# Optimization experiments

Measured on AMD Instinct MI355X. Metric: run time of the kernel, lower is better.

The kernel has to match this reference:

```python
import jax, jax.numpy as jnp
import numpy as np

S = 64   # feature-map height/width = sqrt(qvk_dim)
M = 2    # memory_block_size


def _block_divide(t):
    # (b, c, S*S) -> (b, c, (S/M)**2, M*M), matching
    # Rearrange('b c (h m1) (w m2) -> b c (h w) (m1 m2)')
    b, c, _ = t.shape
    h = S // M
    t = t.reshape(b, c, h, M, h, M)
    t = jnp.transpose(t, (0, 1, 2, 4, 3, 5))
    return t.reshape(b, c, h * h, M * M)


def setup_inputs() -> dict:
    key = jax.random.key(0)
    k1, k2, k3, k4 = jax.random.split(key, 4)
    B, C, F = 64, 64, S * S
    x = jax.random.normal(k1, (B, C, F), dtype=jnp.float32)
    scale = 1.0 / np.sqrt(F)
    Wq = jax.random.normal(k2, (F, F), dtype=jnp.float32) * scale
    Wk = jax.random.normal(k3, (F, F), dtype=jnp.float32) * scale
    Wv = jax.random.normal(k4, (F, F), dtype=jnp.float32) * scale
    return {"x": x, "Wq": Wq, "Wk": Wk, "Wv": Wv}


def reference(x, Wq, Wk, Wv):
    # Linear(in, out, bias=False): y = x @ W.T, W: (out, in)
    q = _block_divide(jnp.einsum('bcf,qf->bcq', x, Wq))  # (b,c,n,g)
    k = _block_divide(jnp.einsum('bcf,qf->bcq', x, Wk))  # (b,c,n,p)
    v = _block_divide(jnp.einsum('bcf,qf->bcq', x, Wv))  # (b,c,n,p)
    # score[b,c,n,g,p] = q[b,c,n,g] * k[b,c,n,p]; softmax over p (dim=4)
    score = q[..., :, None] * k[..., None, :]             # (b,c,n,g,p)
    att = jax.nn.softmax(score, axis=-1)
    # matmul(att (g,p), v (p,1)) -> (g,1), then flatten blocks
    out = jnp.einsum('bcngp,bcnp->bcng', att, v)          # (b,c,n,g)
    b, c, n, g = out.shape
    return out.reshape(b, c, n * g)
```

## Files before the change

### kernel.cpp

```cpp
#include <hip/hip_runtime.h>

#define F        4096
#define NE       ((size_t)F * F)

typedef __attribute__((ext_vector_type(8)))  short bf16x8;
typedef __attribute__((ext_vector_type(4)))  float f32x4;
typedef __attribute__((ext_vector_type(16))) float f32x16;

typedef const void __attribute__((address_space(1)))* gas1p;
typedef void __attribute__((address_space(3)))*       as3p;

__device__ __forceinline__ void gload16(const void* g, void* l) {
    __builtin_amdgcn_global_load_lds((gas1p)g, (as3p)l, 16, 0, 0);
}

__device__ __forceinline__ unsigned short f2bf(float f) {
    union { float f; unsigned int u; } c; c.f = f;
    unsigned int u = c.u;
    u += 0x7fffu + ((u >> 16) & 1u);
    return (unsigned short)(u >> 16);
}
__device__ __forceinline__ float bf2f(unsigned short u) {
    union { unsigned int u; float f; } c; c.u = ((unsigned int)u) << 16;
    return c.f;
}

__global__ void cvt_all(const float* __restrict__ s0, const float* __restrict__ s1,
                        const float* __restrict__ s2, const float* __restrict__ s3,
                        unsigned short* __restrict__ d0, unsigned short* __restrict__ d1,
                        unsigned short* __restrict__ d2, unsigned short* __restrict__ d3,
                        int n4) {
    const float* src = (blockIdx.y == 0) ? s0 : (blockIdx.y == 1) ? s1
                      : (blockIdx.y == 2) ? s2 : s3;
    unsigned short* dst = (blockIdx.y == 0) ? d0 : (blockIdx.y == 1) ? d1
                         : (blockIdx.y == 2) ? d2 : d3;
    int idx    = blockIdx.x * blockDim.x + threadIdx.x;
    int stride = gridDim.x * blockDim.x;
    const float4* in4 = (const float4*)src;
    ushort4* out4 = (ushort4*)dst;
    for (int i = idx; i < n4; i += stride) {
        float4 v = in4[i];
        ushort4 o;
        o.x = f2bf(v.x); o.y = f2bf(v.y); o.z = f2bf(v.z); o.w = f2bf(v.w);
        out4[i] = o;
    }
}

__device__ __forceinline__ int qo_map(int o) {
    int nblk = o >> 2, g = o & 3;
    return (nblk >> 5) * 128 + (g >> 1) * 64 + (nblk & 31) * 2 + (g & 1);
}

#define MFMA16(a, b, c) __builtin_amdgcn_mfma_f32_16x16x32_bf16(a, b, c, 0, 0, 0)
#define MFMA32(a, b, c) __builtin_amdgcn_mfma_f32_32x32x16_bf16(a, b, c, 0, 0, 0)

#define GBM 256
#define GBN 256
#define GBK 32
#define NKT (F / GBK)
#define ELPS (GBM * GBK)

__launch_bounds__(512, 1)
__global__ void gemm_qkv(const unsigned short* __restrict__ Xb,
                         const unsigned short* __restrict__ Qw,
                         const unsigned short* __restrict__ Kw,
                         const unsigned short* __restrict__ Vw,
                         unsigned short* __restrict__ qkv) {
    __shared__ __align__(16) unsigned short Als[4][GBM][GBK];
    __shared__ __align__(16) unsigned short Bls[4][GBN][GBK];

    const int tid  = threadIdx.x;
    const int lane = tid & 63;
    const int wid  = tid >> 6;
    const int wm   = wid >> 2;
    const int wn   = wid & 3;

    const int bid = blockIdx.x;
    const int swz = (bid & 7) * 96 + (bid >> 3);
    const int mt  = swz & 15;
    const int nt  = swz >> 4;
    const int bm  = mt * GBM;
    const int bnG = nt * GBN;
    const int mat = bnG >> 12;
    const int bn  = bnG & 4095;
    const unsigned short* __restrict__ Wsel = (mat == 0) ? Qw : (mat == 1) ? Kw : Vw;

    const int sr_row = tid >> 2;
    const int sr_chn = (tid & 3) ^ ((tid >> 3) & 3) ^ ((tid >> 5) & 3);
    const unsigned short* aSrc0 = Xb + (size_t)(bm + sr_row) * F + sr_chn * 8;
    const unsigned short* aSrc1 = aSrc0 + (size_t)128 * F;
    const unsigned short* bSrc0 = Wsel + (size_t)qo_map(bn + sr_row) * F + sr_chn * 8;
    const unsigned short* bSrc1 = Wsel + (size_t)qo_map(bn + 128 + sr_row) * F + sr_chn * 8;

#define STAGE_A(s, tt) do {                                                     \
        gload16(aSrc0 + (size_t)(tt) * GBK, (void*)&Als[s][wid * 16][0]);       \
        gload16(aSrc1 + (size_t)(tt) * GBK, (void*)&Als[s][128 + wid * 16][0]); \
    } while (0)
#define STAGE_B(s, tt) do {                                                     \
        gload16(bSrc0 + (size_t)(tt) * GBK, (void*)&Bls[s][wid * 16][0]);       \
        gload16(bSrc1 + (size_t)(tt) * GBK, (void*)&Bls[s][128 + wid * 16][0]); \
    } while (0)

    const int lrow = lane & 31;
    const int l5   = lane >> 5;
    const int rx   = ((lrow >> 1) & 3) ^ ((lrow >> 3) & 3);
    const int se0  = ((0 * 2 + l5) ^ rx) * 8;
    const int se1  = ((1 * 2 + l5) ^ rx) * 8;

    const unsigned short* aRow[4];
#pragma unroll
    for (int mi = 0; mi < 4; ++mi)
        aRow[mi] = &Als[0][wm * 128 + mi * 32 + lrow][0];
    const unsigned short* bRow[2];
#pragma unroll
    for (int nj = 0; nj < 2; ++nj)
        bRow[nj] = &Bls[0][wn * 64 + nj * 32 + lrow][0];

    f32x16 acc[4][2];
#pragma unroll
    for (int mi = 0; mi < 4; ++mi)
#pragma unroll
        for (int nj = 0; nj < 2; ++nj)
#pragma unroll
            for (int r = 0; r < 16; ++r)
                acc[mi][nj][r] = 0.f;

    STAGE_A(0, 0); STAGE_B(0, 0);
    STAGE_A(1, 1); STAGE_B(1, 1);
    STAGE_A(2, 2); STAGE_B(2, 2);
    asm volatile("s_waitcnt vmcnt(4)" ::: "memory");
    __builtin_amdgcn_s_barrier();
    __builtin_amdgcn_sched_barrier(0);

    bf16x8 af0[4], af1[4], bf0[2], bf1[2];
#pragma unroll
    for (int mi = 0; mi < 4; ++mi) {
        af0[mi] = *(const bf16x8*)(aRow[mi] + se0);
        af1[mi] = *(const bf16x8*)(aRow[mi] + se1);
    }
#pragma unroll
    for (int nj = 0; nj < 2; ++nj) {
        bf0[nj] = *(const bf16x8*)(bRow[nj] + se0);
        bf1[nj] = *(const bf16x8*)(bRow[nj] + se1);
    }

#pragma unroll 2
    for (int t = 0; t < NKT; ++t) {
        const int sn = (t + 1) & 3;
        const int ss = (t + 3) & 3;
        const int tt = (t + 3) & (NKT - 1);
        const int so = sn * ELPS;

        __builtin_amdgcn_s_setprio(1);
#pragma unroll
        for (int mi = 0; mi < 4; ++mi) {
            acc[mi][0] = MFMA32(af0[mi], bf0[0], acc[mi][0]);
            acc[mi][1] = MFMA32(af0[mi], bf0[1], acc[mi][1]);
            af0[mi] = *(const bf16x8*)(aRow[mi] + so + se0);
        }
        bf0[0] = *(const bf16x8*)(bRow[0] + so + se0);
        bf0[1] = *(const bf16x8*)(bRow[1] + so + se0);
#pragma unroll
        for (int mi = 0; mi < 4; ++mi) {
            acc[mi][0] = MFMA32(af1[mi], bf1[0], acc[mi][0]);
            acc[mi][1] = MFMA32(af1[mi], bf1[1], acc[mi][1]);
            af1[mi] = *(const bf16x8*)(aRow[mi] + so + se1);
        }
        bf1[0] = *(const bf16x8*)(bRow[0] + so + se1);
        bf1[1] = *(const bf16x8*)(bRow[1] + so + se1);
        __builtin_amdgcn_s_setprio(0);

        STAGE_A(ss, tt);
        STAGE_B(ss, tt);
        __builtin_amdgcn_sched_barrier(0);
        asm volatile("s_waitcnt vmcnt(4)" ::: "memory");
        __builtin_amdgcn_sched_barrier(0);
        __builtin_amdgcn_s_barrier();
    }

    asm volatile("s_waitcnt vmcnt(0)" ::: "memory");

    unsigned short* outB = qkv + (size_t)mat * NE;
#pragma unroll
    for (int mi = 0; mi < 4; ++mi) {
#pragma unroll
        for (int nj = 0; nj < 2; ++nj) {
#pragma unroll
            for (int r = 0; r < 16; ++r) {
                int row = bm + wm * 128 + mi * 32 + (r & 3) + 8 * (r >> 2) + 4 * l5;
                int col = bn + wn * 64 + nj * 32 + lrow;
                outB[(size_t)row * F + col] = f2bf(acc[mi][nj][r]);
            }
        }
    }
#undef STAGE_A
#undef STAGE_B
}

__global__ void attn_ep(const unsigned short* __restrict__ qkv,
                        float* __restrict__ out) {
    const size_t NB = NE / 4;
    const ushort4* q4 = (const ushort4*)qkv;
    const ushort4* k4 = q4 + NB;
    const ushort4* v4 = k4 + NB;
    float4* o4 = (float4*)out;
    size_t i      = (size_t)blockIdx.x * blockDim.x + threadIdx.x;
    size_t stride = (size_t)gridDim.x * blockDim.x;
    for (; i < NB; i += stride) {
        ushort4 qu = q4[i], ku = k4[i], vu = v4[i];
        float q0 = bf2f(qu.x), q1 = bf2f(qu.y), q2 = bf2f(qu.z), q3 = bf2f(qu.w);
        float k0 = bf2f(ku.x), k1 = bf2f(ku.y), k2 = bf2f(ku.z), k3 = bf2f(ku.w);
        float v0 = bf2f(vu.x), v1 = bf2f(vu.y), v2 = bf2f(vu.z), v3 = bf2f(vu.w);
        float4 res;
#pragma unroll
        for (int g = 0; g < 4; ++g) {
            float qg = (g == 0) ? q0 : (g == 1) ? q1 : (g == 2) ? q2 : q3;
            float s0 = qg * k0, s1 = qg * k1, s2 = qg * k2, s3 = qg * k3;
            float mx = fmaxf(fmaxf(s0, s1), fmaxf(s2, s3));
            float e0 = __expf(s0 - mx), e1 = __expf(s1 - mx);
            float e2 = __expf(s2 - mx), e3 = __expf(s3 - mx);
            float num = e0 * v0 + e1 * v1 + e2 * v2 + e3 * v3;
            float den = e0 + e1 + e2 + e3;
            float r = num / den;
            if (g == 0) res.x = r; else if (g == 1) res.y = r;
            else if (g == 2) res.z = r; else res.w = r;
        }
        o4[i] = res;
    }
}

#define BM       128
#define BN       128
#define BK       32
#define NTHREADS 512
#define KTILES   (F / BK)

__launch_bounds__(NTHREADS, 1)
__global__ void fused_qkv_attn(const unsigned short* __restrict__ Xb,
                               const unsigned short* __restrict__ Qw,
                               const unsigned short* __restrict__ Kw,
                               const unsigned short* __restrict__ Vw,
                               float* __restrict__ out) {
    __shared__ __align__(16) unsigned short Alds[BM][BK];
    __shared__ __align__(16) unsigned short Blds[3][BN][BK];

    const int tid  = threadIdx.x;
    const int lane = tid & 63;
    const int wid  = tid >> 6;
    const int wm   = wid >> 1;
    const int wn   = wid & 1;

    const int bm = blockIdx.y * BM;
    const int bn = blockIdx.x * BN;

    const int srow   = wid * 16 + (lane >> 2);
    const int kchunk = (lane & 3) ^ ((lane >> 3) & 3);
    const int scol   = kchunk * 8;

    const unsigned short* aG = Xb + (size_t)(bm + srow) * F + scol;
    const int o  = bn + srow;
    const int qo = qo_map(o);
    const unsigned short* qG = Qw + (size_t)qo * F + scol;
    const unsigned short* kG = Kw + (size_t)qo * F + scol;
    const unsigned short* vG = Vw + (size_t)qo * F + scol;

    unsigned short* aL = &Alds[wid * 16][0];
    unsigned short* qL = &Blds[0][wid * 16][0];
    unsigned short* kL = &Blds[1][wid * 16][0];
    unsigned short* vL = &Blds[2][wid * 16][0];

    const int fr  = lane & 15;
    const int fq  = lane >> 4;
    const int fq2 = fq ^ ((fr >> 1) & 3);

    const unsigned short* aP[2];
#pragma unroll
    for (int m = 0; m < 2; ++m)
        aP[m] = &Alds[wm * 32 + m * 16 + fr][fq2 * 8];
    const unsigned short* bP[4];
#pragma unroll
    for (int n = 0; n < 4; ++n)
        bP[n] = &Blds[0][wn * 64 + n * 16 + fr][fq2 * 8];

    f32x4 acc[3][2][4];
#pragma unroll
    for (int t = 0; t < 3; ++t)
#pragma unroll
        for (int m = 0; m < 2; ++m)
#pragma unroll
            for (int n = 0; n < 4; ++n)
                acc[t][m][n] = (f32x4){0.f, 0.f, 0.f, 0.f};

    for (int kt = 0; kt < KTILES; ++kt) {
        gload16(aG, aL);
        gload16(qG, qL);
        gload16(kG, kL);
        gload16(vG, vL);
        aG += BK; qG += BK; kG += BK; vG += BK;
        __syncthreads();

        bf16x8 afr[2];
#pragma unroll
        for (int m = 0; m < 2; ++m)
            afr[m] = *(const bf16x8*)aP[m];

#pragma unroll
        for (int t = 0; t < 3; ++t) {
#pragma unroll
            for (int n = 0; n < 4; ++n) {
                bf16x8 bfr = *(const bf16x8*)(bP[n] + t * (BN * BK));
#pragma unroll
                for (int m = 0; m < 2; ++m)
                    acc[t][m][n] = MFMA16(afr[m], bfr, acc[t][m][n]);
            }
        }
        __syncthreads();
    }

#pragma unroll
    for (int m = 0; m < 2; ++m) {
#pragma unroll
        for (int n = 0; n < 4; ++n) {
#pragma unroll
            for (int r = 0; r < 4; ++r) {
                float q  = acc[0][m][n][r];
                float k0 = acc[1][m][n][r];
                float v0 = acc[2][m][n][r];
                float k1 = __shfl_xor(k0, 1);
                float k2 = __shfl_xor(k0, 2);
                float k3 = __shfl_xor(k0, 3);
                float v1 = __shfl_xor(v0, 1);
                float v2 = __shfl_xor(v0, 2);
                float v3 = __shfl_xor(v0, 3);
                float s0 = q * k0, s1 = q * k1, s2 = q * k2, s3 = q * k3;
                float mx = fmaxf(fmaxf(s0, s1), fmaxf(s2, s3));
                float e0 = __expf(s0 - mx), e1 = __expf(s1 - mx);
                float e2 = __expf(s2 - mx), e3 = __expf(s3 - mx);
                float num = e0 * v0 + e1 * v1 + e2 * v2 + e3 * v3;
                float den = e0 + e1 + e2 + e3;
                int row = bm + wm * 32 + m * 16 + fq * 4 + r;
                int oc  = bn + wn * 64 + n * 16 + fr;
                out[(size_t)row * F + oc] = num / den;
            }
        }
    }
}

extern "C" void kernel_launch(void* const* d_in, const int* in_sizes, int n_in,
                              void* d_out, int out_size, void* d_ws, size_t ws_size,
                              hipStream_t stream) {
    const float* x  = (const float*)d_in[0];
    const float* Wq = (const float*)d_in[1];
    const float* Wk = (const float*)d_in[2];
    const float* Wv = (const float*)d_in[3];
    float* out = (float*)d_out;

    unsigned short* xb  = (unsigned short*)d_ws;
    unsigned short* wqb = xb  + NE;
    unsigned short* wkb = wqb + NE;
    unsigned short* wvb = wkb + NE;
    unsigned short* qkv = wvb + NE;

    const int n4 = (int)(NE / 4);
    cvt_all<<<dim3(2048, 4), 256, 0, stream>>>(x, Wq, Wk, Wv, xb, wqb, wkb, wvb, n4);

    const size_t need_fast = NE * 2 * 7;
    if (ws_size >= need_fast) {
        gemm_qkv<<<768, 512, 0, stream>>>(xb, wqb, wkb, wvb, qkv);
        attn_ep<<<4096, 256, 0, stream>>>(qkv, out);
    } else {
        dim3 grid(F / BN, F / BM);
        fused_qkv_attn<<<grid, NTHREADS, 0, stream>>>(xb, wqb, wkb, wvb, out);
    }
}
```

Measured before the change: 471.0 us.

## Reorganize LDS staging to k-chunk-major layout instead of XOR-swizzled rows

Result: slower. 697.7 us (+48.1%).

```diff
diff --git a/kernel.cpp b/kernel.cpp
--- a/kernel.cpp
+++ b/kernel.cpp
@@ -54,11 +54,9 @@
 #define MFMA16(a, b, c) __builtin_amdgcn_mfma_f32_16x16x32_bf16(a, b, c, 0, 0, 0)
 #define MFMA32(a, b, c) __builtin_amdgcn_mfma_f32_32x32x16_bf16(a, b, c, 0, 0, 0)
 
-#define GBM 256
-#define GBN 256
 #define GBK 32
 #define NKT (F / GBK)
-#define ELPS (GBM * GBK)
+#define SLT 8192
 
 __launch_bounds__(512, 1)
 __global__ void gemm_qkv(const unsigned short* __restrict__ Xb,
@@ -66,8 +64,8 @@
                          const unsigned short* __restrict__ Kw,
                          const unsigned short* __restrict__ Vw,
                          unsigned short* __restrict__ qkv) {
-    __shared__ __align__(16) unsigned short Als[4][GBM][GBK];
-    __shared__ __align__(16) unsigned short Bls[4][GBN][GBK];
+    __shared__ __align__(16) unsigned short AlsF[4 * SLT];
+    __shared__ __align__(16) unsigned short BlsF[4 * SLT];
 
     const int tid  = threadIdx.x;
     const int lane = tid & 63;
@@ -79,42 +77,33 @@
     const int swz = (bid & 7) * 96 + (bid >> 3);
     const int mt  = swz & 15;
     const int nt  = swz >> 4;
-    const int bm  = mt * GBM;
-    const int bnG = nt * GBN;
+    const int bm  = mt * 256;
+    const int bnG = nt * 256;
     const int mat = bnG >> 12;
     const int bn  = bnG & 4095;
     const unsigned short* __restrict__ Wsel = (mat == 0) ? Qw : (mat == 1) ? Kw : Vw;
 
-    const int sr_row = tid >> 2;
-    const int sr_chn = (tid & 3) ^ ((tid >> 3) & 3) ^ ((tid >> 5) & 3);
-    const unsigned short* aSrc0 = Xb + (size_t)(bm + sr_row) * F + sr_chn * 8;
-    const unsigned short* aSrc1 = aSrc0 + (size_t)128 * F;
-    const unsigned short* bSrc0 = Wsel + (size_t)qo_map(bn + sr_row) * F + sr_chn * 8;
-    const unsigned short* bSrc1 = Wsel + (size_t)qo_map(bn + 128 + sr_row) * F + sr_chn * 8;
-
-#define STAGE_A(s, tt) do {                                                     \
-        gload16(aSrc0 + (size_t)(tt) * GBK, (void*)&Als[s][wid * 16][0]);       \
-        gload16(aSrc1 + (size_t)(tt) * GBK, (void*)&Als[s][128 + wid * 16][0]); \
+    const int srow = tid & 255;
+    const int skc1 = tid >> 8;
+    const unsigned short* aS1 = Xb + (size_t)(bm + srow) * F + skc1 * 8;
+    const unsigned short* aS2 = aS1 + 16;
+    const int qrow = qo_map(bn + srow);
+    const unsigned short* bS1 = Wsel + (size_t)qrow * F + skc1 * 8;
+    const unsigned short* bS2 = bS1 + 16;
+
+#define STAGE_A(s, tt) do {                                                      \
+        gload16(aS1 + (size_t)(tt) * GBK, (void*)&AlsF[(s) * SLT + wid * 512]);  \
+        gload16(aS2 + (size_t)(tt) * GBK, (void*)&AlsF[(s) * SLT + 4096 + wid * 512]); \
     } while (0)
-#define STAGE_B(s, tt) do {                                                     \
-        gload16(bSrc0 + (size_t)(tt) * GBK, (void*)&Bls[s][wid * 16][0]);       \
-        gload16(bSrc1 + (size_t)(tt) * GBK, (void*)&Bls[s][128 + wid * 16][0]); \
+#define STAGE_B(s, tt) do {                                                      \
+        gload16(bS1 + (size_t)(tt) * GBK, (void*)&BlsF[(s) * SLT + wid * 512]);  \
+        gload16(bS2 + (size_t)(tt) * GBK, (void*)&BlsF[(s) * SLT + 4096 + wid * 512]); \
     } while (0)
 
     const int lrow = lane & 31;
     const int l5   = lane >> 5;
-    const int rx   = ((lrow >> 1) & 3) ^ ((lrow >> 3) & 3);
-    const int se0  = ((0 * 2 + l5) ^ rx) * 8;
-    const int se1  = ((1 * 2 + l5) ^ rx) * 8;
-
-    const unsigned short* aRow[4];
-#pragma unroll
-    for (int mi = 0; mi < 4; ++mi)
-        aRow[mi] = &Als[0][wm * 128 + mi * 32 + lrow][0];
-    const unsigned short* bRow[2];
-#pragma unroll
-    for (int nj = 0; nj < 2; ++nj)
-        bRow[nj] = &Bls[0][wn * 64 + nj * 32 + lrow][0];
+    const unsigned short* aRd = &AlsF[l5 * 2048 + (wm * 128 + lrow) * 8];
+    const unsigned short* bRd = &BlsF[l5 * 2048 + (wn * 64 + lrow) * 8];
 
     f32x16 acc[4][2];
 #pragma unroll
@@ -135,13 +124,13 @@
     bf16x8 af0[4], af1[4], bf0[2], bf1[2];
 #pragma unroll
     for (int mi = 0; mi < 4; ++mi) {
-        af0[mi] = *(const bf16x8*)(aRow[mi] + se0);
-        af1[mi] = *(const bf16x8*)(aRow[mi] + se1);
+        af0[mi] = *(const bf16x8*)(aRd + mi * 256);
+        af1[mi] = *(const bf16x8*)(aRd + 4096 + mi * 256);
     }
 #pragma unroll
     for (int nj = 0; nj < 2; ++nj) {
-        bf0[nj] = *(const bf16x8*)(bRow[nj] + se0);
-        bf1[nj] = *(const bf16x8*)(bRow[nj] + se1);
+        bf0[nj] = *(const bf16x8*)(bRd + nj * 256);
+        bf1[nj] = *(const bf16x8*)(bRd + 4096 + nj * 256);
     }
 
 #pragma unroll 2
@@ -149,25 +138,25 @@
         const int sn = (t + 1) & 3;
         const int ss = (t + 3) & 3;
         const int tt = (t + 3) & (NKT - 1);
-        const int so = sn * ELPS;
+        const int so = sn * SLT;
 
         __builtin_amdgcn_s_setprio(1);
 #pragma unroll
         for (int mi = 0; mi < 4; ++mi) {
             acc[mi][0] = MFMA32(af0[mi], bf0[0], acc[mi][0]);
             acc[mi][1] = MFMA32(af0[mi], bf0[1], acc[mi][1]);
-            af0[mi] = *(const bf16x8*)(aRow[mi] + so + se0);
-        }
-        bf0[0] = *(const bf16x8*)(bRow[0] + so + se0);
-        bf0[1] = *(const bf16x8*)(bRow[1] + so + se0);
+            af0[mi] = *(const bf16x8*)(aRd + so + mi * 256);
+        }
+        bf0[0] = *(const bf16x8*)(bRd + so + 0 * 256);
+        bf0[1] = *(const bf16x8*)(bRd + so + 1 * 256);
 #pragma unroll
         for (int mi = 0; mi < 4; ++mi) {
             acc[mi][0] = MFMA32(af1[mi], bf1[0], acc[mi][0]);
             acc[mi][1] = MFMA32(af1[mi], bf1[1], acc[mi][1]);
-            af1[mi] = *(const bf16x8*)(aRow[mi] + so + se1);
-        }
-        bf1[0] = *(const bf16x8*)(bRow[0] + so + se1);
-        bf1[1] = *(const bf16x8*)(bRow[1] + so + se1);
+            af1[mi] = *(const bf16x8*)(aRd + so + 4096 + mi * 256);
+        }
+        bf1[0] = *(const bf16x8*)(bRd + so + 4096 + 0 * 256);
+        bf1[1] = *(const bf16x8*)(bRd + so + 4096 + 1 * 256);
         __builtin_amdgcn_s_setprio(0);
 
         STAGE_A(ss, tt);
```
